# Kernel tuning notes

Hardware: AMD Instinct MI355X
Metric: run time of the kernel (lower is better)

## Reference

```python
import jax, jax.numpy as jnp
import numpy as np

D = 1024      # d_model
H = 16        # num_heads
DH = D // H   # head_dim = 64
BASE = 10000.0


def setup_inputs() -> dict:
    key = jax.random.key(0)
    ks = jax.random.split(key, 5)
    lengths = np.array([1024, 768, 896, 1024], dtype=np.int32)
    cu = np.concatenate([[0], np.cumsum(lengths)]).astype(np.int32)
    T = int(cu[-1])  # 3712 packed tokens
    x = jax.random.normal(ks[0], (T, D), dtype=jnp.float32)
    Wqkv = jax.random.normal(ks[1], (D, 3 * D), dtype=jnp.float32) / np.sqrt(D)
    bqkv = jax.random.normal(ks[2], (3 * D,), dtype=jnp.float32) * 0.02
    Wo = jax.random.normal(ks[3], (D, D), dtype=jnp.float32) / np.sqrt(D)
    bo = jax.random.normal(ks[4], (D,), dtype=jnp.float32) * 0.02
    return {"x": x, "Wqkv": Wqkv, "bqkv": bqkv, "Wo": Wo, "bo": bo,
            "cu_seqlens": jnp.asarray(cu), "max_seqlen": 1024}


def reference(x, Wqkv, bqkv, Wo, bo, cu_seqlens, max_seqlen):
    T = x.shape[0]
    B = cu_seqlens.shape[0] - 1
    S = int(max_seqlen)

    # fused qkv projection: [T, 3, H, DH]
    qkv = (x @ Wqkv + bqkv).reshape(T, 3, H, DH)
    q, k, v = qkv[:, 0], qkv[:, 1], qkv[:, 2]

    # per-token sequence id and within-sequence position (RoPE resets per seq)
    tok = jnp.arange(T)
    seq_id = jnp.searchsorted(cu_seqlens, tok, side='right') - 1  # [T]
    pos = tok - cu_seqlens[seq_id]                                # [T]

    # RoPE, non-interleaved (rotate-half over full head_dim)
    inv_freq = 1.0 / (BASE ** (jnp.arange(0, DH, 2, dtype=jnp.float32) / DH))
    ang = pos[:, None].astype(jnp.float32) * inv_freq             # [T, DH/2]
    cos = jnp.cos(ang)[:, None, :]                                # [T, 1, DH/2]
    sin = jnp.sin(ang)[:, None, :]

    def rope(t):
        t1, t2 = t[..., : DH // 2], t[..., DH // 2:]
        return jnp.concatenate([t1 * cos - t2 * sin, t2 * cos + t1 * sin], axis=-1)

    q, k = rope(q), rope(k)

    # scatter packed tokens into padded [B, S, H, DH] (varlen attention)
    qp = jnp.zeros((B, S, H, DH), x.dtype).at[seq_id, pos].set(q)
    kp = jnp.zeros((B, S, H, DH), x.dtype).at[seq_id, pos].set(k)
    vp = jnp.zeros((B, S, H, DH), x.dtype).at[seq_id, pos].set(v)
    valid = jnp.zeros((B, S), bool).at[seq_id, pos].set(True)

    scale = 1.0 / np.sqrt(DH)
    scores = jnp.einsum('bqhd,bkhd->bhqk', qp, kp) * scale        # [B,H,S,S]
    causal = jnp.tril(jnp.ones((S, S), bool))
    mask = causal[None, None] & valid[:, None, None, :]
    scores = jnp.where(mask, scores, jnp.asarray(-1e30, scores.dtype))
    attn = jax.nn.softmax(scores, axis=-1)
    op = jnp.einsum('bhqk,bkhd->bqhd', attn, vp)                  # [B,S,H,DH]

    # unpad back to packed layout, then output projection (W_o)
    out = op[seq_id, pos].reshape(T, D)
    return out @ Wo + bo
```

## Files before the change

### kernel.cpp

```cpp
#include <hip/hip_runtime.h>

typedef _Float16 f16;
typedef _Float16 f16x8 __attribute__((ext_vector_type(8)));
typedef _Float16 f16x4 __attribute__((ext_vector_type(4)));
typedef float f32x4 __attribute__((ext_vector_type(4)));

#define BM 128
#define BN 128
#define BKK 32

#define MFMA16(a, b, c) __builtin_amdgcn_mfma_f32_16x16x32_f16((a), (b), (c), 0, 0, 0)

typedef __attribute__((address_space(3))) void lds_void;
typedef const __attribute__((address_space(1))) void g_void;
__device__ __forceinline__ void async_copy16(void* lds, const void* g) {
    __builtin_amdgcn_global_load_lds((g_void*)g, (lds_void*)lds, 16, 0, 0);
}

__global__ __launch_bounds__(256) void prep(
    const float* __restrict__ x, f16* __restrict__ xh, int T,
    const float* __restrict__ Wqkv, const float* __restrict__ Wo,
    f16* __restrict__ wqkvT, f16* __restrict__ woT,
    float2* __restrict__ tab, int Spad) {
    int id = blockIdx.x;
    int tid = threadIdx.x;
    if (id < 1024) {
        __shared__ f16 tile[64][65];
        const float* in; f16* out; int N, bx, by;
        if (id < 768) { in = Wqkv; out = wqkvT; N = 3072; bx = id % 48; by = id / 48; }
        else { int j = id - 768; in = Wo; out = woT; N = 1024; bx = j % 16; by = j / 16; }
        const int K = 1024;
        int n0 = bx * 64, k0 = by * 64;
        int c = tid & 63, rb = tid >> 6;
#pragma unroll
        for (int it = 0; it < 16; ++it) {
            int r = rb + it * 4;
            tile[r][c] = (f16)in[(size_t)(k0 + r) * N + n0 + c];
        }
        __syncthreads();
#pragma unroll
        for (int it = 0; it < 16; ++it) {
            int rr = rb + it * 4;
            out[(size_t)(n0 + rr) * K + k0 + c] = tile[c][rr];
        }
    } else if (id < 1152) {
        int idx = (id - 1024) * 256 + tid;
        if (idx < Spad * 32) {
            int pos = idx >> 5, i = idx & 31;
            float inv = exp2f((float)i * (-13.287712379549449f / 32.f));
            float sn, cs;
            __sincosf((float)pos * inv, &sn, &cs);
            tab[idx] = make_float2(cs, sn);
        }
    } else {
        int i4 = ((id - 1152) * 256 + tid) * 4;
        if (i4 < T * 1024) {
            float4 v = *reinterpret_cast<const float4*>(x + i4);
            f16x4 o;
            o[0] = (f16)v.x; o[1] = (f16)v.y; o[2] = (f16)v.z; o[3] = (f16)v.w;
            *reinterpret_cast<f16x4*>(xh + i4) = o;
        }
    }
}

__device__ __forceinline__ void gemm_core(
    const f16* __restrict__ A, const f16* __restrict__ Bt,
    int M, int N, int K, int bx, int by, int tid,
    f16 lA[2][BM * BKK], f16 lB[2][BN * BKK], f32x4 acc[4][4]) {
    int lane = tid & 63, w = tid >> 6;
    int lr = lane & 15, lg = lane >> 4;
    int wm = (w & 1) * 64, wn = (w >> 1) * 64;
    int srow = tid >> 2;
    int scol = (tid & 3) * 8;
    const f16* ga0 = A  + (size_t)min(by * BM + srow,      M - 1) * K + scol;
    const f16* ga1 = A  + (size_t)min(by * BM + 64 + srow, M - 1) * K + scol;
    const f16* gb0 = Bt + (size_t)min(bx * BN + srow,      N - 1) * K + scol;
    const f16* gb1 = Bt + (size_t)min(bx * BN + 64 + srow, N - 1) * K + scol;
    int NT = K / BKK;
#define STAGE(curb, kt) do {                                        \
        int ko = (kt) * BKK;                                        \
        async_copy16(&lA[curb][w * 512],        ga0 + ko);          \
        async_copy16(&lA[curb][2048 + w * 512], ga1 + ko);          \
        async_copy16(&lB[curb][w * 512],        gb0 + ko);          \
        async_copy16(&lB[curb][2048 + w * 512], gb1 + ko);          \
    } while (0)
    STAGE(0, 0);
    __syncthreads();
    int cur = 0;
    for (int kt = 0; kt < NT; ++kt) {
        if (kt + 1 < NT) STAGE(cur ^ 1, kt + 1);
        f16x8 af[4], bf[4];
#pragma unroll
        for (int i = 0; i < 4; ++i) {
            af[i] = *reinterpret_cast<const f16x8*>(&lA[cur][(wm + i * 16 + lr) * BKK + lg * 8]);
            bf[i] = *reinterpret_cast<const f16x8*>(&lB[cur][(wn + i * 16 + lr) * BKK + lg * 8]);
        }
#pragma unroll
        for (int mi = 0; mi < 4; ++mi)
#pragma unroll
            for (int ni = 0; ni < 4; ++ni)
                acc[mi][ni] = MFMA16(af[mi], bf[ni], acc[mi][ni]);
        __syncthreads();
        cur ^= 1;
    }
#undef STAGE
}

__global__ __launch_bounds__(256) void gemm_qkv(
    const f16* __restrict__ A, const f16* __restrict__ Bt,
    const float* __restrict__ bias, const int* __restrict__ cu,
    const float2* __restrict__ tab, int M, int Bn, int Spad,
    f16* __restrict__ qh2, f16* __restrict__ kh2, f16* __restrict__ vt, int nbx) {
    __shared__ f16 lA[2][BM * BKK];
    __shared__ f16 lB[2][BN * BKK];
    int tid = threadIdx.x;
    int nwg = gridDim.x, wg = blockIdx.x;
    int tile = ((nwg & 7) == 0) ? ((wg & 7) * (nwg >> 3) + (wg >> 3)) : wg;
    int by = tile / nbx, bx = tile % nbx;

    f32x4 acc[4][4] = {};
    gemm_core(A, Bt, M, 3072, 1024, bx, by, tid, lA, lB, acc);

    int lane = tid & 63, w = tid >> 6;
    int lr = lane & 15, lg = lane >> 4;
    int wm = (w & 1) * 64, wn = (w >> 1) * 64;
    int colwave = bx * BN + wn;
    int sect = colwave >> 10;
    int h = (colwave & 1023) >> 6;
    float bv[4];
#pragma unroll
    for (int ni = 0; ni < 4; ++ni) bv[ni] = bias[colwave + ni * 16 + lr];

#pragma unroll
    for (int mi = 0; mi < 4; ++mi) {
        int row0 = by * BM + wm + mi * 16 + 4 * lg;
        if (row0 >= M) continue;
        if (sect == 2) {
            int b0 = 0, p0 = row0;
            for (int q = 0; q < Bn; ++q) {
                int lo = cu[q], hi = cu[q + 1];
                if (row0 >= lo && row0 < hi) { b0 = q; p0 = row0 - lo; break; }
            }
            bool pack = (row0 + 3 < M) && ((p0 & 3) == 0) && (row0 + 3 < cu[b0 + 1]);
            if (pack) {
                size_t vb = (size_t)(b0 * 16 + h) * 64;
#pragma unroll
                for (int ni = 0; ni < 4; ++ni) {
                    int d = ni * 16 + lr;
                    f16x4 ov;
#pragma unroll
                    for (int r = 0; r < 4; ++r) ov[r] = (f16)(acc[mi][ni][r] + bv[ni]);
                    *reinterpret_cast<f16x4*>(vt + (vb + d) * Spad + p0) = ov;
                }
            } else {
                for (int r = 0; r < 4; ++r) {
                    int row = row0 + r;
                    if (row >= M) break;
                    int b = 0, pos = row;
                    for (int q = 0; q < Bn; ++q) {
                        int lo = cu[q], hi = cu[q + 1];
                        if (row >= lo && row < hi) { b = q; pos = row - lo; break; }
                    }
                    size_t vb = (size_t)(b * 16 + h) * 64;
#pragma unroll
                    for (int ni = 0; ni < 4; ++ni)
                        vt[(vb + ni * 16 + lr) * Spad + pos] = (f16)(acc[mi][ni][r] + bv[ni]);
                }
            }
        } else {
            float sc = sect == 0 ? 0.125f : 1.f;
            f16* dstbase = sect == 0 ? qh2 : kh2;
            for (int r = 0; r < 4; ++r) {
                int row = row0 + r;
                if (row >= M) break;
                int b = 0, pos = row;
                for (int q = 0; q < Bn; ++q) {
                    int lo = cu[q], hi = cu[q + 1];
                    if (row >= lo && row < hi) { b = q; pos = row - lo; break; }
                }
                const float2* tb = tab + pos * 32;
                f16* dst = dstbase + ((size_t)(b * 16 + h) * Spad + pos) * 64;
#pragma unroll
                for (int p = 0; p < 2; ++p) {
                    int i = p * 16 + lr;
                    float2 csn = tb[i];
                    float v1 = acc[mi][p][r] + bv[p];
                    float v2 = acc[mi][p + 2][r] + bv[p + 2];
                    dst[i]      = (f16)((v1 * csn.x - v2 * csn.y) * sc);
                    dst[i + 32] = (f16)((v2 * csn.x + v1 * csn.y) * sc);
                }
            }
        }
    }
}

__global__ __launch_bounds__(256) void gemm_out(
    const f16* __restrict__ A, const f16* __restrict__ Bt,
    const float* __restrict__ bias, float* __restrict__ Cf,
    int M, int N, int K, int nbx) {
    __shared__ f16 lA[2][BM * BKK];
    __shared__ f16 lB[2][BN * BKK];
    int tid = threadIdx.x;
    int nwg = gridDim.x, wg = blockIdx.x;
    int tile = ((nwg & 7) == 0) ? ((wg & 7) * (nwg >> 3) + (wg >> 3)) : wg;
    int by = tile / nbx, bx = tile % nbx;

    f32x4 acc[4][4] = {};
    gemm_core(A, Bt, M, N, K, bx, by, tid, lA, lB, acc);

    int lane = tid & 63, w = tid >> 6;
    int lr = lane & 15, lg = lane >> 4;
    int wm = (w & 1) * 64, wn = (w >> 1) * 64;
#pragma unroll
    for (int mi = 0; mi < 4; ++mi) {
#pragma unroll
        for (int ni = 0; ni < 4; ++ni) {
            int col = bx * BN + wn + ni * 16 + lr;
            float bvv = bias[col];
#pragma unroll
            for (int r = 0; r < 4; ++r) {
                int row = by * BM + wm + mi * 16 + 4 * lg + r;
                if (row >= M) continue;
                Cf[(size_t)row * N + col] = acc[mi][ni][r] + bvv;
            }
        }
    }
}

__global__ __launch_bounds__(128) void attn_fwd(
    const f16* __restrict__ qh2, const f16* __restrict__ kh2,
    const f16* __restrict__ vt, const int* __restrict__ cu,
    f16* __restrict__ oh, int Spad, int nq, int Bn) {
    int wgid = blockIdx.x;
    int nbh = Bn * 16;
    int b, h, qi;
    if ((nbh & 7) == 0) {
        int xcd = wgid & 7, rest = wgid >> 3, nbh8 = nbh >> 3;
        int bhhi = rest % nbh8;
        qi = (nq - 1) - rest / nbh8;
        int bhv = (bhhi << 3) | xcd;
        b = bhv >> 4; h = bhv & 15;
    } else {
        qi = wgid % nq;
        int bhv = wgid / nq;
        b = bhv >> 4; h = bhv & 15;
    }
    int bh = b * 16 + h;
    int s0 = cu[b];
    int len = cu[b + 1] - s0;
    int q0 = qi * 32;
    if (q0 >= len) return;
    int tid = threadIdx.x;
    int wv = tid >> 6;
    int lane = tid & 63, lr = lane & 15, lg = lane >> 4;
    __shared__ f16 pl[2][2][16][40];
    __shared__ float mlb[2][2][16];
    __shared__ f32x4 owb[2][4][16][4];

    const f16* qbase = qh2 + (size_t)bh * Spad * 64;
    const f16* kbase = kh2 + (size_t)bh * Spad * 64;
    const f16* vbase = vt  + (size_t)bh * 64 * Spad;

    f16x8 qf[2][2];
#pragma unroll
    for (int qt = 0; qt < 2; ++qt) {
        const f16* qp = qbase + (size_t)(q0 + 16 * qt + lr) * 64 + 8 * lg;
        qf[qt][0] = *reinterpret_cast<const f16x8*>(qp);
        qf[qt][1] = *reinterpret_cast<const f16x8*>(qp + 32);
    }
    float mrun[2] = {-1e30f, -1e30f}, lrun[2] = {0.f, 0.f};
    f32x4 oacc[2][4] = {};

    int kend = min(q0 + 32, len);
    int ntk = (kend + 31) >> 5;

    f16x8 kf[2][2], kn[2][2];
#pragma unroll
    for (int j = 0; j < 2; ++j) {
        const f16* kp = kbase + (size_t)(wv * 32 + 16 * j + lr) * 64 + 8 * lg;
        kf[j][0] = *reinterpret_cast<const f16x8*>(kp);
        kf[j][1] = *reinterpret_cast<const f16x8*>(kp + 32);
    }

    for (int kt = wv; kt < ntk; kt += 2) {
        int kk0 = kt << 5;
        f16x8 vf[4];
#pragma unroll
        for (int dt = 0; dt < 4; ++dt)
            vf[dt] = *reinterpret_cast<const f16x8*>(
                vbase + (size_t)(16 * dt + lr) * Spad + kk0 + 8 * lg);
        f32x4 st[2][2];
#pragma unroll
        for (int qt = 0; qt < 2; ++qt)
#pragma unroll
            for (int j = 0; j < 2; ++j) {
                f32x4 z = {0, 0, 0, 0};
                z = MFMA16(kf[j][0], qf[qt][0], z);
                z = MFMA16(kf[j][1], qf[qt][1], z);
                st[qt][j] = z;
            }
        if (kt + 2 < ntk) {
#pragma unroll
            for (int j = 0; j < 2; ++j) {
                const f16* kp = kbase + (size_t)(kk0 + 64 + 16 * j + lr) * 64 + 8 * lg;
                kn[j][0] = *reinterpret_cast<const f16x8*>(kp);
                kn[j][1] = *reinterpret_cast<const f16x8*>(kp + 32);
            }
        }
#pragma unroll
        for (int qt = 0; qt < 2; ++qt) {
            int qr = q0 + 16 * qt + lr;
            float sv[2][4];
            float mx = -1e30f;
#pragma unroll
            for (int j = 0; j < 2; ++j)
#pragma unroll
                for (int r = 0; r < 4; ++r) {
                    int kc = kk0 + 16 * j + 4 * lg + r;
                    float v = st[qt][j][r];
                    if (kc > qr || kc >= len) v = -1e30f;
                    sv[j][r] = v;
                    mx = fmaxf(mx, v);
                }
            mx = fmaxf(mx, __shfl_xor(mx, 16, 64));
            mx = fmaxf(mx, __shfl_xor(mx, 32, 64));
            float mnew = fmaxf(mrun[qt], mx);
            float al = __expf(mrun[qt] - mnew);
            mrun[qt] = mnew;
            float rs = 0.f;
            f16x4 pk0, pk1;
#pragma unroll
            for (int r = 0; r < 4; ++r) {
                float p0 = __expf(sv[0][r] - mnew);
                float p1 = __expf(sv[1][r] - mnew);
                rs += p0 + p1;
                pk0[r] = (f16)p0;
                pk1[r] = (f16)p1;
            }
            rs += __shfl_xor(rs, 16, 64);
            rs += __shfl_xor(rs, 32, 64);
            lrun[qt] = lrun[qt] * al + rs;
            *reinterpret_cast<f16x4*>(&pl[wv][qt][lr][4 * lg])      = pk0;
            *reinterpret_cast<f16x4*>(&pl[wv][qt][lr][16 + 4 * lg]) = pk1;
#pragma unroll
            for (int dt = 0; dt < 4; ++dt)
#pragma unroll
                for (int r = 0; r < 4; ++r) oacc[qt][dt][r] *= al;
        }
        asm volatile("s_waitcnt lgkmcnt(0)" ::: "memory");
        __builtin_amdgcn_sched_barrier(0);
        f16x8 pa0 = *reinterpret_cast<const f16x8*>(&pl[wv][0][lr][8 * lg]);
        f16x8 pa1 = *reinterpret_cast<const f16x8*>(&pl[wv][1][lr][8 * lg]);
#pragma unroll
        for (int dt = 0; dt < 4; ++dt) {
            oacc[0][dt] = MFMA16(vf[dt], pa0, oacc[0][dt]);
            oacc[1][dt] = MFMA16(vf[dt], pa1, oacc[1][dt]);
        }
        asm volatile("" ::: "memory");
#pragma unroll
        for (int j = 0; j < 2; ++j) {
            kf[j][0] = kn[j][0];
            kf[j][1] = kn[j][1];
        }
    }

    if (wv == 1) {
#pragma unroll
        for (int qt = 0; qt < 2; ++qt) {
            if (lg == 0) { mlb[qt][0][lr] = mrun[qt]; mlb[qt][1][lr] = lrun[qt]; }
#pragma unroll
            for (int dt = 0; dt < 4; ++dt)
                owb[qt][dt][lr][lg] = oacc[qt][dt];
        }
    }
    __syncthreads();
    if (wv == 0) {
#pragma unroll
        for (int qt = 0; qt < 2; ++qt) {
            int qr = q0 + 16 * qt + lr;
            if (qr >= len) continue;
            float m1 = mlb[qt][0][lr], l1 = mlb[qt][1][lr];
            float mnew = fmaxf(mrun[qt], m1);
            float a0 = __expf(mrun[qt] - mnew);
            float a1 = __expf(m1 - mnew);
            float linv = 1.f / (lrun[qt] * a0 + l1 * a1);
            f16* orow = oh + (size_t)(s0 + qr) * 1024 + h * 64;
#pragma unroll
            for (int dt = 0; dt < 4; ++dt) {
                f32x4 o1 = owb[qt][dt][lr][lg];
                f16x4 ov;
#pragma unroll
                for (int r = 0; r < 4; ++r)
                    ov[r] = (f16)((oacc[qt][dt][r] * a0 + o1[r] * a1) * linv);
                *reinterpret_cast<f16x4*>(orow + 16 * dt + 4 * lg) = ov;
            }
        }
    }
}

extern "C" void kernel_launch(void* const* d_in, const int* in_sizes, int n_in,
                              void* d_out, int out_size, void* d_ws, size_t ws_size,
                              hipStream_t stream) {
    const float* x    = (const float*)d_in[0];
    const float* Wqkv = (const float*)d_in[1];
    const float* bqkv = (const float*)d_in[2];
    const float* Wo   = (const float*)d_in[3];
    const float* bo   = (const float*)d_in[4];
    const int*   cu   = (const int*)d_in[5];

    const int Dm = 1024;
    int T  = in_sizes[0] / Dm;
    int Bn = in_sizes[5] - 1;
    int Spad = 1024;

    auto al = [](size_t v) { return (v + 255) & ~(size_t)255; };
    char* w = (char*)d_ws;
    size_t off = 0;
    f16* xh     = (f16*)(w + off); off = al(off + (size_t)2 * T * 1024);
    f16* wqkvT  = (f16*)(w + off); off = al(off + (size_t)2 * 3072 * 1024);
    f16* woT    = (f16*)(w + off); off = al(off + (size_t)2 * 1024 * 1024);
    f16* qh2    = (f16*)(w + off); off = al(off + (size_t)2 * Bn * 16 * 64 * (size_t)Spad);
    f16* kh2    = (f16*)(w + off); off = al(off + (size_t)2 * Bn * 16 * 64 * (size_t)Spad);
    f16* vtp    = (f16*)(w + off); off = al(off + (size_t)2 * Bn * 16 * 64 * (size_t)Spad);
    f16* ohp    = (f16*)(w + off); off = al(off + (size_t)2 * T * 1024);
    float2* tab = (float2*)(w + off); off = al(off + (size_t)8 * Spad * 32);
    (void)ws_size;

    prep<<<1152 + T, 256, 0, stream>>>(x, xh, T, Wqkv, Wo, wqkvT, woT, tab, Spad);
    {
        int nbx = 3072 / BN, nby = (T + BM - 1) / BM;
        gemm_qkv<<<nbx * nby, 256, 0, stream>>>(xh, wqkvT, bqkv, cu, tab,
                                                T, Bn, Spad, qh2, kh2, vtp, nbx);
    }
    {
        int nq = Spad / 32;
        int ngrid = nq * 16 * Bn;
        attn_fwd<<<ngrid, 128, 0, stream>>>(qh2, kh2, vtp, cu, ohp, Spad, nq, Bn);
    }
    {
        int nbx = 1024 / BN, nby = (T + BM - 1) / BM;
        gemm_out<<<nbx * nby, 256, 0, stream>>>(ohp, woT, bo, (float*)d_out,
                                                T, 1024, 1024, nbx);
    }
}
```

Baseline: 125.3 us.

## Split attention keys across four waves and precompute token batch/position table

The attention kernel now runs four waves per query tile instead of two. Each wave strides over key tiles by four, and the partial softmax statistics and outputs from waves 1-3 are merged by wave 0 through shared memory. The aim is more parallelism for short query tiles and less serial key-loop latency, at the cost of more LDS and a heavier merge step. Separately, prep now computes a packed (batch, position) per token, so the QKV GEMM epilogue loads it instead of scanning cu_seqlens.

```diff
diff --git a/kernel.cpp b/kernel.cpp
--- a/kernel.cpp
+++ b/kernel.cpp
@@ -21,7 +21,8 @@
     const float* __restrict__ x, f16* __restrict__ xh, int T,
     const float* __restrict__ Wqkv, const float* __restrict__ Wo,
     f16* __restrict__ wqkvT, f16* __restrict__ woT,
-    float2* __restrict__ tab, int Spad) {
+    float2* __restrict__ tab, int Spad,
+    const int* __restrict__ cu, int Bn, int* __restrict__ bpos) {
     int id = blockIdx.x;
     int tid = threadIdx.x;
     if (id < 1024) {
@@ -52,13 +53,23 @@
             __sincosf((float)pos * inv, &sn, &cs);
             tab[idx] = make_float2(cs, sn);
         }
-    } else {
+    } else if (id < 1152 + T) {
         int i4 = ((id - 1152) * 256 + tid) * 4;
         if (i4 < T * 1024) {
             float4 v = *reinterpret_cast<const float4*>(x + i4);
             f16x4 o;
             o[0] = (f16)v.x; o[1] = (f16)v.y; o[2] = (f16)v.z; o[3] = (f16)v.w;
             *reinterpret_cast<f16x4*>(xh + i4) = o;
+        }
+    } else {
+        int t = (id - 1152 - T) * 256 + tid;
+        if (t < T) {
+            int b = 0, pos = t;
+            for (int q = 0; q < Bn; ++q) {
+                int lo = cu[q], hi = cu[q + 1];
+                if (t >= lo && t < hi) { b = q; pos = t - lo; break; }
+            }
+            bpos[t] = (b << 16) | pos;
         }
     }
 }
@@ -108,8 +119,8 @@
 
 __global__ __launch_bounds__(256) void gemm_qkv(
     const f16* __restrict__ A, const f16* __restrict__ Bt,
-    const float* __restrict__ bias, const int* __restrict__ cu,
-    const float2* __restrict__ tab, int M, int Bn, int Spad,
+    const float* __restrict__ bias, const int* __restrict__ bpos,
+    const float2* __restrict__ tab, int M, int Spad,
     f16* __restrict__ qh2, f16* __restrict__ kh2, f16* __restrict__ vt, int nbx) {
     __shared__ f16 lA[2][BM * BKK];
     __shared__ f16 lB[2][BN * BKK];
@@ -136,12 +147,9 @@
         int row0 = by * BM + wm + mi * 16 + 4 * lg;
         if (row0 >= M) continue;
         if (sect == 2) {
-            int b0 = 0, p0 = row0;
-            for (int q = 0; q < Bn; ++q) {
-                int lo = cu[q], hi = cu[q + 1];
-                if (row0 >= lo && row0 < hi) { b0 = q; p0 = row0 - lo; break; }
-            }
-            bool pack = (row0 + 3 < M) && ((p0 & 3) == 0) && (row0 + 3 < cu[b0 + 1]);
+            int v0 = bpos[row0];
+            int b0 = v0 >> 16, p0 = v0 & 0xffff;
+            bool pack = (row0 + 3 < M) && ((p0 & 3) == 0) && ((bpos[row0 + 3] >> 16) == b0);
             if (pack) {
                 size_t vb = (size_t)(b0 * 16 + h) * 64;
 #pragma unroll
@@ -156,11 +164,8 @@
                 for (int r = 0; r < 4; ++r) {
                     int row = row0 + r;
                     if (row >= M) break;
-                    int b = 0, pos = row;
-                    for (int q = 0; q < Bn; ++q) {
-                        int lo = cu[q], hi = cu[q + 1];
-                        if (row >= lo && row < hi) { b = q; pos = row - lo; break; }
-                    }
+                    int v = bpos[row];
+                    int b = v >> 16, pos = v & 0xffff;
                     size_t vb = (size_t)(b * 16 + h) * 64;
 #pragma unroll
                     for (int ni = 0; ni < 4; ++ni)
@@ -173,11 +178,8 @@
             for (int r = 0; r < 4; ++r) {
                 int row = row0 + r;
                 if (row >= M) break;
-                int b = 0, pos = row;
-                for (int q = 0; q < Bn; ++q) {
-                    int lo = cu[q], hi = cu[q + 1];
-                    if (row >= lo && row < hi) { b = q; pos = row - lo; break; }
-                }
+                int v = bpos[row];
+                int b = v >> 16, pos = v & 0xffff;
                 const float2* tb = tab + pos * 32;
                 f16* dst = dstbase + ((size_t)(b * 16 + h) * Spad + pos) * 64;
 #pragma unroll
@@ -227,7 +229,7 @@
     }
 }
 
-__global__ __launch_bounds__(128) void attn_fwd(
+__global__ __launch_bounds__(256) void attn_fwd(
     const f16* __restrict__ qh2, const f16* __restrict__ kh2,
     const f16* __restrict__ vt, const int* __restrict__ cu,
     f16* __restrict__ oh, int Spad, int nq, int Bn) {
@@ -253,9 +255,9 @@
     int tid = threadIdx.x;
     int wv = tid >> 6;
     int lane = tid & 63, lr = lane & 15, lg = lane >> 4;
-    __shared__ f16 pl[2][2][16][40];
-    __shared__ float mlb[2][2][16];
-    __shared__ f32x4 owb[2][4][16][4];
+    __shared__ f16 pl[4][2][16][40];
+    __shared__ float mlb[3][2][2][16];
+    __shared__ f32x4 owb[3][2][4][16][4];
 
     const f16* qbase = qh2 + (size_t)bh * Spad * 64;
     const f16* kbase = kh2 + (size_t)bh * Spad * 64;
@@ -282,7 +284,7 @@
         kf[j][1] = *reinterpret_cast<const f16x8*>(kp + 32);
     }
 
-    for (int kt = wv; kt < ntk; kt += 2) {
+    for (int kt = wv; kt < ntk; kt += 4) {
         int kk0 = kt << 5;
         f16x8 vf[4];
 #pragma unroll
@@ -299,10 +301,10 @@
                 z = MFMA16(kf[j][1], qf[qt][1], z);
                 st[qt][j] = z;
             }
-        if (kt + 2 < ntk) {
+        if (kt + 4 < ntk) {
 #pragma unroll
             for (int j = 0; j < 2; ++j) {
-                const f16* kp = kbase + (size_t)(kk0 + 64 + 16 * j + lr) * 64 + 8 * lg;
+                const f16* kp = kbase + (size_t)(kk0 + 128 + 16 * j + lr) * 64 + 8 * lg;
                 kn[j][0] = *reinterpret_cast<const f16x8*>(kp);
                 kn[j][1] = *reinterpret_cast<const f16x8*>(kp + 32);
             }
@@ -364,13 +366,16 @@
         }
     }
 
-    if (wv == 1) {
+    if (wv > 0) {
 #pragma unroll
         for (int qt = 0; qt < 2; ++qt) {
-            if (lg == 0) { mlb[qt][0][lr] = mrun[qt]; mlb[qt][1][lr] = lrun[qt]; }
+            if (lg == 0) {
+                mlb[wv - 1][qt][0][lr] = mrun[qt];
+                mlb[wv - 1][qt][1][lr] = lrun[qt];
+            }
 #pragma unroll
             for (int dt = 0; dt < 4; ++dt)
-                owb[qt][dt][lr][lg] = oacc[qt][dt];
+                owb[wv - 1][qt][dt][lr][lg] = oacc[qt][dt];
         }
     }
     __syncthreads();
@@ -379,19 +384,29 @@
         for (int qt = 0; qt < 2; ++qt) {
             int qr = q0 + 16 * qt + lr;
             if (qr >= len) continue;
-            float m1 = mlb[qt][0][lr], l1 = mlb[qt][1][lr];
-            float mnew = fmaxf(mrun[qt], m1);
-            float a0 = __expf(mrun[qt] - mnew);
-            float a1 = __expf(m1 - mnew);
-            float linv = 1.f / (lrun[qt] * a0 + l1 * a1);
+            float m = mrun[qt];
+#pragma unroll
+            for (int i = 0; i < 3; ++i) m = fmaxf(m, mlb[i][qt][0][lr]);
+            float a0 = __expf(mrun[qt] - m);
+            float lsum = lrun[qt] * a0;
+            float ai[3];
+#pragma unroll
+            for (int i = 0; i < 3; ++i) {
+                ai[i] = __expf(mlb[i][qt][0][lr] - m);
+                lsum += mlb[i][qt][1][lr] * ai[i];
+            }
+            float linv = 1.f / lsum;
             f16* orow = oh + (size_t)(s0 + qr) * 1024 + h * 64;
 #pragma unroll
             for (int dt = 0; dt < 4; ++dt) {
-                f32x4 o1 = owb[qt][dt][lr][lg];
                 f16x4 ov;
 #pragma unroll
-                for (int r = 0; r < 4; ++r)
-                    ov[r] = (f16)((oacc[qt][dt][r] * a0 + o1[r] * a1) * linv);
+                for (int r = 0; r < 4; ++r) {
+                    float o = oacc[qt][dt][r] * a0;
+#pragma unroll
+                    for (int i = 0; i < 3; ++i) o += owb[i][qt][dt][lr][lg][r] * ai[i];
+                    ov[r] = (f16)(o * linv);
+                }
                 *reinterpret_cast<f16x4*>(orow + 16 * dt + 4 * lg) = ov;
             }
         }
@@ -424,18 +439,23 @@
     f16* vtp    = (f16*)(w + off); off = al(off + (size_t)2 * Bn * 16 * 64 * (size_t)Spad);
     f16* ohp    = (f16*)(w + off); off = al(off + (size_t)2 * T * 1024);
     float2* tab = (float2*)(w + off); off = al(off + (size_t)8 * Spad * 32);
+    int* bpos   = (int*)(w + off);   off = al(off + (size_t)4 * T);
     (void)ws_size;
 
-    prep<<<1152 + T, 256, 0, stream>>>(x, xh, T, Wqkv, Wo, wqkvT, woT, tab, Spad);
+    {
+        int nb = 1152 + T + (T + 255) / 256;
+        prep<<<nb, 256, 0, stream>>>(x, xh, T, Wqkv, Wo, wqkvT, woT, tab, Spad,
+                                     cu, Bn, bpos);
+    }
     {
         int nbx = 3072 / BN, nby = (T + BM - 1) / BM;
-        gemm_qkv<<<nbx * nby, 256, 0, stream>>>(xh, wqkvT, bqkv, cu, tab,
-                                                T, Bn, Spad, qh2, kh2, vtp, nbx);
+        gemm_qkv<<<nbx * nby, 256, 0, stream>>>(xh, wqkvT, bqkv, bpos, tab,
+                                                T, Spad, qh2, kh2, vtp, nbx);
     }
     {
         int nq = Spad / 32;
         int ngrid = nq * 16 * Bn;
-        attn_fwd<<<ngrid, 128, 0, stream>>>(qh2, kh2, vtp, cu, ohp, Spad, nq, Bn);
+        attn_fwd<<<ngrid, 256, 0, stream>>>(qh2, kh2, vtp, cu, ohp, Spad, nq, Bn);
     }
     {
         int nbx = 1024 / BN, nby = (T + BM - 1) / BM;
```

After: 119.8 us. 1.05x faster.
